# Kernel tuning notes

Measured on AMD Instinct MI355X. Metric: run time of the kernel, lower is better.

The kernel has to match this reference:

```python
import jax, jax.numpy as jnp
import numpy as np

B, S, D = 1, 4096, 768
H = 12
HD = D // H  # 64


def setup_inputs() -> dict:
    key = jax.random.key(0)
    ks = jax.random.split(key, 6)
    sc = 1.0 / np.sqrt(D)
    return {
        "x": jax.random.normal(ks[0], (B, S, D), dtype=jnp.float32),
        "wq": jax.random.normal(ks[1], (D, D), dtype=jnp.float32) * sc,
        "wk": jax.random.normal(ks[2], (D, D), dtype=jnp.float32) * sc,
        "wv": jax.random.normal(ks[3], (D, D), dtype=jnp.float32) * sc,
        "wo": jax.random.normal(ks[4], (D, D), dtype=jnp.float32) * sc,
        "bo": jax.random.normal(ks[5], (D,), dtype=jnp.float32) * 0.02,
    }


def reference(x, wq, wk, wv, wo, bo):
    b, n, _ = x.shape
    # projections (torch Linear: x @ W.T; here weights stored as (d_in, d_out))
    q = (x @ wq).reshape(b, n, H, HD).transpose(0, 2, 1, 3)  # b h n d
    k = (x @ wk).reshape(b, n, H, HD).transpose(0, 2, 1, 3)
    v = (x @ wv).reshape(b, n, H, HD).transpose(0, 2, 1, 3)
    scores = jnp.einsum("bhqd,bhkd->bhqk", q, k)
    causal = jnp.tril(jnp.ones((n, n), dtype=bool))  # True = keep
    scores = jnp.where(causal, scores, -jnp.inf)
    weights = jax.nn.softmax(scores / np.sqrt(HD), axis=-1)
    ctx = jnp.einsum("bhqk,bhkd->bhqd", weights, v)
    ctx = ctx.transpose(0, 2, 1, 3).reshape(b, n, D)
    return ctx @ wo + bo
```

## Files before the change

### kernel.cpp

```cpp
#include <hip/hip_runtime.h>


typedef short bf16x8 __attribute__((ext_vector_type(8)));
typedef float f32x4 __attribute__((ext_vector_type(4)));
typedef unsigned short u16;

static constexpr int S_LEN = 4096;
static constexpr int DIM   = 768;
static constexpr int NH    = 12;
static constexpr float QSCALE = 0.125f * 1.44269504088896340736f;

__device__ inline u16 f2bf(float f) {
  union { float f; unsigned int u; } v; v.f = f;
  unsigned int r = v.u + 0x7FFFu + ((v.u >> 16) & 1u);
  return (u16)(r >> 16);
}

__device__ inline void gload_lds16(const u16* g, u16* s) {
  __builtin_amdgcn_global_load_lds(
      (const __attribute__((address_space(1))) unsigned int*)g,
      (__attribute__((address_space(3))) unsigned int*)s, 16, 0, 0);
}

__global__ __launch_bounds__(256)
void prep_kernel(const float* __restrict__ x, const float* __restrict__ w0,
                 const float* __restrict__ w1, const float* __restrict__ w2,
                 const float* __restrict__ w3, u16* __restrict__ xb,
                 u16* __restrict__ t0, u16* __restrict__ t1,
                 u16* __restrict__ t2, u16* __restrict__ t3) {
  if (blockIdx.z == 4) {
    const size_t n = (size_t)S_LEN * DIM;
    const int id = blockIdx.y * 12 + blockIdx.x;
    const size_t stride = (size_t)144 * 256 * 8;
    for (size_t i = ((size_t)id * 256 + threadIdx.x) * 8; i < n; i += stride) {
      const float4 a = *(const float4*)(x + i);
      const float4 b = *(const float4*)(x + i + 4);
      bf16x8 o;
      o[0] = (short)f2bf(a.x); o[1] = (short)f2bf(a.y);
      o[2] = (short)f2bf(a.z); o[3] = (short)f2bf(a.w);
      o[4] = (short)f2bf(b.x); o[5] = (short)f2bf(b.y);
      o[6] = (short)f2bf(b.z); o[7] = (short)f2bf(b.w);
      *(bf16x8*)(xb + i) = o;
    }
    return;
  }
  __shared__ float T[64][65];
  const float* src; u16* dst;
  switch (blockIdx.z) {
    case 0: src = w0; dst = t0; break;
    case 1: src = w1; dst = t1; break;
    case 2: src = w2; dst = t2; break;
    default: src = w3; dst = t3; break;
  }
  const int k0 = blockIdx.y * 64, n0 = blockIdx.x * 64;
  const int r = threadIdx.x >> 2, c0 = (threadIdx.x & 3) * 16;
#pragma unroll
  for (int i = 0; i < 4; ++i) {
    const float4 v = *(const float4*)(src + (size_t)(k0 + r) * DIM + n0 + c0 + i * 4);
    T[r][c0 + i * 4 + 0] = v.x;
    T[r][c0 + i * 4 + 1] = v.y;
    T[r][c0 + i * 4 + 2] = v.z;
    T[r][c0 + i * 4 + 3] = v.w;
  }
  __syncthreads();
  bf16x8 o0, o1;
#pragma unroll
  for (int i = 0; i < 8; ++i) {
    o0[i] = (short)f2bf(T[c0 + i][r]);
    o1[i] = (short)f2bf(T[c0 + 8 + i][r]);
  }
  *(bf16x8*)(dst + (size_t)(n0 + r) * DIM + k0 + c0) = o0;
  *(bf16x8*)(dst + (size_t)(n0 + r) * DIM + k0 + c0 + 8) = o1;
}

template <int MODE>
__global__ __launch_bounds__(256)
void mfma_gemm_kernel(const u16* __restrict__ A, const u16* __restrict__ Bq,
                      const u16* __restrict__ Bk, const u16* __restrict__ Bv,
                      const float* __restrict__ bias, u16* __restrict__ Qb,
                      u16* __restrict__ Kb, u16* __restrict__ VT,
                      float* __restrict__ Out) {
  constexpr int MT = (MODE == 0) ? 4 : 2;
  constexpr int BM = MT * 32;
  __shared__ __align__(16) u16 Al[BM * 64];
  __shared__ __align__(16) u16 Bl[96 * 64];

  const int tid  = threadIdx.x;
  const int wv   = tid >> 6;
  const int lane = tid & 63;
  const int quad = lane >> 4;
  const int l16  = lane & 15;
  const int wr = wv >> 1, wc = wv & 1;
  const int m0 = blockIdx.y * BM;
  const int n0 = blockIdx.x * 96;

  int wi = 0, nb = n0;
  const u16* BT = Bq;
  if (MODE == 0) {
    wi = n0 / DIM;
    nb = n0 - wi * DIM;
    BT = (wi == 0) ? Bq : (wi == 1) ? Bk : Bv;
  }

  const int sr8 = lane >> 3;
  const int sc  = ((lane & 7) ^ sr8) * 8;
  const int key = l16 & 7;

  const bool swp = (MODE == 1) || (wi < 2);

  f32x4 acc[MT][3] = {};

  for (int k0 = 0; k0 < DIM; k0 += 64) {
    __syncthreads();
#pragma unroll
    for (int j = 0; j < MT; ++j)
      gload_lds16(A + (size_t)(m0 + wv * (BM / 4) + j * 8 + sr8) * DIM + k0 + sc,
                  &Al[(wv * (BM / 4) + j * 8) * 64]);
#pragma unroll
    for (int j = 0; j < 3; ++j)
      gload_lds16(BT + (size_t)(nb + wv * 24 + j * 8 + sr8) * DIM + k0 + sc,
                  &Bl[(wv * 24 + j * 8) * 64]);
    __syncthreads();

#pragma unroll
    for (int kh = 0; kh < 2; ++kh) {
      const int cb = kh * 4;
      bf16x8 af[MT], bfr[3];
#pragma unroll
      for (int mt = 0; mt < MT; ++mt) {
        const int row = wr * (BM / 2) + mt * 16 + l16;
        af[mt] = *(const bf16x8*)&Al[row * 64 + ((cb + quad) ^ key) * 8];
      }
#pragma unroll
      for (int nt = 0; nt < 3; ++nt) {
        const int row = wc * 48 + nt * 16 + l16;
        bfr[nt] = *(const bf16x8*)&Bl[row * 64 + ((cb + quad) ^ key) * 8];
      }
      if (swp) {
#pragma unroll
        for (int mt = 0; mt < MT; ++mt)
#pragma unroll
          for (int nt = 0; nt < 3; ++nt)
            acc[mt][nt] = __builtin_amdgcn_mfma_f32_16x16x32_bf16(
                bfr[nt], af[mt], acc[mt][nt], 0, 0, 0);
      } else {
#pragma unroll
        for (int mt = 0; mt < MT; ++mt)
#pragma unroll
          for (int nt = 0; nt < 3; ++nt)
            acc[mt][nt] = __builtin_amdgcn_mfma_f32_16x16x32_bf16(
                af[mt], bfr[nt], acc[mt][nt], 0, 0, 0);
      }
    }
  }

  if (MODE == 0 && wi >= 2) {
#pragma unroll
    for (int mt = 0; mt < MT; ++mt) {
#pragma unroll
      for (int nt = 0; nt < 3; ++nt) {
        const int row  = m0 + wr * (BM / 2) + mt * 16 + quad * 4;
        const int ncol = nb + wc * 48 + nt * 16 + l16;
        u16 pk[4];
#pragma unroll
        for (int r = 0; r < 4; ++r) pk[r] = f2bf(acc[mt][nt][r]);
        unsigned long long v;
        __builtin_memcpy(&v, pk, 8);
        *(unsigned long long*)(VT + (size_t)ncol * S_LEN + row) = v;
      }
    }
  } else if (MODE == 0) {
    u16* dst = (wi == 0) ? Qb : Kb;
    const float sc_out = (wi == 0) ? QSCALE : 1.0f;
#pragma unroll
    for (int mt = 0; mt < MT; ++mt) {
#pragma unroll
      for (int nt = 0; nt < 3; ++nt) {
        const int row = m0 + wr * (BM / 2) + mt * 16 + l16;
        const int ncb = nb + wc * 48 + nt * 16 + quad * 4;
        u16 pk[4];
#pragma unroll
        for (int r = 0; r < 4; ++r) pk[r] = f2bf(acc[mt][nt][r] * sc_out);
        unsigned long long v;
        __builtin_memcpy(&v, pk, 8);
        *(unsigned long long*)(dst + (size_t)row * DIM + ncb) = v;
      }
    }
  } else {
#pragma unroll
    for (int mt = 0; mt < MT; ++mt) {
#pragma unroll
      for (int nt = 0; nt < 3; ++nt) {
        const int row = m0 + wr * (BM / 2) + mt * 16 + l16;
        const int ncb = n0 + wc * 48 + nt * 16 + quad * 4;
        const float4 b4 = *(const float4*)(bias + ncb);
        float4 ov;
        ov.x = acc[mt][nt][0] + b4.x;
        ov.y = acc[mt][nt][1] + b4.y;
        ov.z = acc[mt][nt][2] + b4.z;
        ov.w = acc[mt][nt][3] + b4.w;
        *(float4*)(Out + (size_t)row * DIM + ncb) = ov;
      }
    }
  }
}

__global__ __launch_bounds__(256)
void attn_mfma_kernel(const u16* __restrict__ Qb, const u16* __restrict__ Kb,
                      const u16* __restrict__ VTb, u16* __restrict__ ctx) {
  __shared__ __align__(16) u16 KVl[128 * 64 + 64 * 128];

  u16* Kl = KVl;
  u16* Vl = KVl + 128 * 64;

  const int tid  = threadIdx.x;
  const int w    = tid >> 6;
  const int lane = tid & 63;
  const int quad = lane >> 4;
  const int l16  = lane & 15;
  const int qw   = w >> 1;
  const int kw   = w & 1;
  const int key  = l16 & 7;

  const int id = blockIdx.x;
  const int rc = id & 7, slot = id >> 3;
  const int h  = (slot < 64) ? rc : 8 + (rc >> 1);
  const int bx = (slot < 64) ? slot : ((rc & 1) * 32 + (slot - 64));

  const int sr8  = lane >> 3;
  const int scK  = ((lane & 7) ^ sr8) * 8;
  const int sr16 = lane >> 4;

#pragma unroll 1
  for (int side = 0; side < 2; ++side) {
    const int qt = side ? (127 - bx) : bx;
    const int q0 = qt * 32;

    const u16* qptr = Qb + (size_t)(q0 + qw * 16 + l16) * DIM + h * 64 + quad * 8;
    const bf16x8 aq0 = *(const bf16x8*)(qptr);
    const bf16x8 aq1 = *(const bf16x8*)(qptr + 32);

    f32x4 o[4] = {};
    float l_s = 0.f;
    const int qg = q0 + qw * 16 + l16;

    const int nkt = qt / 2 + 1;
    const int niter = (nkt + 1) >> 1;
    const int my_last = nkt - 1;

#pragma unroll 1
    for (int i = 0; i < niter; ++i) {
      const int k0g = i * 128;
      __syncthreads();
#pragma unroll
      for (int j = 0; j < 4; ++j)
        gload_lds16(Kb + (size_t)(k0g + w * 32 + j * 8 + sr8) * DIM + h * 64 + scK,
                    &Kl[(w * 32 + j * 8) * 64]);
#pragma unroll
      for (int j = 0; j < 4; ++j) {
        const int vrow = w * 16 + j * 4 + sr16;
        const int vcol = ((lane & 15) ^ (vrow & 7)) * 8;
        gload_lds16(VTb + (size_t)(h * 64 + vrow) * S_LEN + k0g + vcol,
                    &Vl[(w * 16 + j * 4) * 128]);
      }
      __syncthreads();

      const int kt_w = 2 * i + kw;
      if (kt_w < nkt) {
        f32x4 s[4];
#pragma unroll
        for (int t = 0; t < 4; ++t) {
          const int row = kw * 64 + t * 16 + l16;
          const bf16x8 bk0 = *(const bf16x8*)&Kl[row * 64 + (quad ^ key) * 8];
          const bf16x8 bk1 = *(const bf16x8*)&Kl[row * 64 + ((quad ^ 4) ^ key) * 8];
          s[t] = __builtin_amdgcn_mfma_f32_16x16x32_bf16(
              bk0, aq0, f32x4{0.f, 0.f, 0.f, 0.f}, 0, 0, 0);
          s[t] = __builtin_amdgcn_mfma_f32_16x16x32_bf16(bk1, aq1, s[t], 0, 0, 0);
        }

        unsigned Wt[4][2];
        if (kt_w == my_last) {
#pragma unroll
          for (int t = 0; t < 4; ++t) {
            float pr[4];
#pragma unroll
            for (int r = 0; r < 4; ++r) {
              const int kvg = k0g + kw * 64 + t * 16 + quad * 4 + r;
              float p = __builtin_amdgcn_exp2f(s[t][r]);
              if (kvg > qg) p = 0.f;
              l_s += p;
              pr[r] = p;
            }
            asm("v_cvt_pk_bf16_f32 %0, %1, %2" : "=v"(Wt[t][0]) : "v"(pr[0]), "v"(pr[1]));
            asm("v_cvt_pk_bf16_f32 %0, %1, %2" : "=v"(Wt[t][1]) : "v"(pr[2]), "v"(pr[3]));
          }
        } else {
#pragma unroll
          for (int t = 0; t < 4; ++t) {
            float pr[4];
#pragma unroll
            for (int r = 0; r < 4; ++r) {
              const float p = __builtin_amdgcn_exp2f(s[t][r]);
              l_s += p;
              pr[r] = p;
            }
            asm("v_cvt_pk_bf16_f32 %0, %1, %2" : "=v"(Wt[t][0]) : "v"(pr[0]), "v"(pr[1]));
            asm("v_cvt_pk_bf16_f32 %0, %1, %2" : "=v"(Wt[t][1]) : "v"(pr[2]), "v"(pr[3]));
          }
        }

        bf16x8 pa0, pa1;
        {
          unsigned a0 = Wt[0][0], b0 = Wt[1][0];
          unsigned a1 = Wt[0][1], b1 = Wt[1][1];
          asm("v_permlane32_swap_b32 %0, %1" : "+v"(a0), "+v"(b0));
          asm("v_permlane16_swap_b32 %0, %1" : "+v"(a0), "+v"(b0));
          asm("v_permlane32_swap_b32 %0, %1" : "+v"(a1), "+v"(b1));
          asm("v_permlane16_swap_b32 %0, %1" : "+v"(a1), "+v"(b1));
          union { unsigned u[4]; bf16x8 v; } U0;
          U0.u[0] = a0; U0.u[1] = a1; U0.u[2] = b0; U0.u[3] = b1;
          pa0 = U0.v;
          unsigned c0 = Wt[2][0], d0 = Wt[3][0];
          unsigned c1 = Wt[2][1], d1 = Wt[3][1];
          asm("v_permlane32_swap_b32 %0, %1" : "+v"(c0), "+v"(d0));
          asm("v_permlane16_swap_b32 %0, %1" : "+v"(c0), "+v"(d0));
          asm("v_permlane32_swap_b32 %0, %1" : "+v"(c1), "+v"(d1));
          asm("v_permlane16_swap_b32 %0, %1" : "+v"(c1), "+v"(d1));
          union { unsigned u[4]; bf16x8 v; } U1;
          U1.u[0] = c0; U1.u[1] = c1; U1.u[2] = d0; U1.u[3] = d1;
          pa1 = U1.v;
        }

#pragma unroll
        for (int t = 0; t < 4; ++t) {
          const int row = t * 16 + l16;
          const int cc0 = (kw * 8 + quad) ^ key;
          const int cc1 = (kw * 8 + quad + 4) ^ key;
          const bf16x8 vb0 = *(const bf16x8*)&Vl[row * 128 + cc0 * 8];
          const bf16x8 vb1 = *(const bf16x8*)&Vl[row * 128 + cc1 * 8];
          o[t] = __builtin_amdgcn_mfma_f32_16x16x32_bf16(pa0, vb0, o[t], 0, 0, 0);
          o[t] = __builtin_amdgcn_mfma_f32_16x16x32_bf16(pa1, vb1, o[t], 0, 0, 0);
        }
      }
    }

    __syncthreads();
    float* Obuf  = (float*)KVl;
    float* lbufF = Obuf + 5120;
#pragma unroll
    for (int t = 0; t < 4; ++t)
      *(f32x4*)&Obuf[(w * 64 + lane) * 20 + t * 4] = o[t];
    lbufF[w * 64 + lane] = l_s;
    __syncthreads();
#pragma unroll
    for (int t = 0; t < 4; ++t) {
      const f32x4 po = *(const f32x4*)&Obuf[((w ^ 1) * 64 + lane) * 20 + t * 4];
      o[t] += po;
    }
    l_s += lbufF[(w ^ 1) * 64 + lane];

    if (kw == 0) {
      float L = l_s;
      L += __shfl_xor(L, 16);
      L += __shfl_xor(L, 32);
#pragma unroll
      for (int r = 0; r < 4; ++r) {
        const float inv = 1.f / __shfl(L, quad * 4 + r);
        const int row = q0 + qw * 16 + quad * 4 + r;
#pragma unroll
        for (int t = 0; t < 4; ++t)
          ctx[(size_t)row * DIM + h * 64 + t * 16 + l16] = f2bf(o[t][r] * inv);
      }
    }
  }
}

extern "C" void kernel_launch(void* const* d_in, const int* in_sizes, int n_in,
                              void* d_out, int out_size, void* d_ws,
                              size_t ws_size, hipStream_t stream) {
  const float* x  = (const float*)d_in[0];
  const float* wq = (const float*)d_in[1];
  const float* wk = (const float*)d_in[2];
  const float* wv = (const float*)d_in[3];
  const float* wo = (const float*)d_in[4];
  const float* bo = (const float*)d_in[5];

  const size_t n_x = (size_t)S_LEN * DIM;
  const size_t n_w = (size_t)DIM * DIM;
  u16* xb  = (u16*)d_ws;
  u16* wtq = xb + n_x;
  u16* wtk = wtq + n_w;
  u16* wtv = wtk + n_w;
  u16* wto = wtv + n_w;
  u16* Qb  = wto + n_w;
  u16* Kb  = Qb + n_x;
  u16* VTb = Kb + n_x;
  u16* ctx = VTb + n_x;

  prep_kernel<<<dim3(12, 12, 5), 256, 0, stream>>>(
      x, wq, wk, wv, wo, xb, wtq, wtk, wtv, wto);

  mfma_gemm_kernel<0><<<dim3(24, 32), 256, 0, stream>>>(
      xb, wtq, wtk, wtv, nullptr, Qb, Kb, VTb, nullptr);

  attn_mfma_kernel<<<dim3(768), 256, 0, stream>>>(Qb, Kb, VTb, ctx);

  mfma_gemm_kernel<1><<<dim3(8, 64), 256, 0, stream>>>(
      ctx, wto, nullptr, nullptr, bo, nullptr, nullptr, nullptr, (float*)d_out);
}
```

Baseline: 169.1 us.

## Double-buffer K tiles in LDS and prefetch next tile during compute

The attention kernel now keeps two K buffers in LDS and issues the global-to-LDS loads for the next K tile before computing the current one. It replaces __syncthreads with explicit waitcnt plus barrier, waiting only for the current tile's loads via vmcnt(4). It also raises wave priority around the MFMA section. This aims to hide K load latency at the cost of more LDS, which may lower occupancy, and it relies on hand-counted vmcnt values. V is still single-buffered.

```diff
diff --git a/kernel.cpp b/kernel.cpp
--- a/kernel.cpp
+++ b/kernel.cpp
@@ -208,10 +208,8 @@
 __global__ __launch_bounds__(256)
 void attn_mfma_kernel(const u16* __restrict__ Qb, const u16* __restrict__ Kb,
                       const u16* __restrict__ VTb, u16* __restrict__ ctx) {
-  __shared__ __align__(16) u16 KVl[128 * 64 + 64 * 128];
-
-  u16* Kl = KVl;
-  u16* Vl = KVl + 128 * 64;
+  __shared__ __align__(16) u16 KVl[2 * 128 * 64 + 64 * 128];
+  u16* const Vl = KVl + 2 * 128 * 64;
 
   const int tid  = threadIdx.x;
   const int w    = tid >> 6;
@@ -251,11 +249,16 @@
 #pragma unroll 1
     for (int i = 0; i < niter; ++i) {
       const int k0g = i * 128;
-      __syncthreads();
-#pragma unroll
-      for (int j = 0; j < 4; ++j)
-        gload_lds16(Kb + (size_t)(k0g + w * 32 + j * 8 + sr8) * DIM + h * 64 + scK,
-                    &Kl[(w * 32 + j * 8) * 64]);
+      asm volatile("s_waitcnt lgkmcnt(0)" ::: "memory");
+      __builtin_amdgcn_s_barrier();
+
+      u16* const kcur = KVl + (i & 1) * (128 * 64);
+      if (i == 0) {
+#pragma unroll
+        for (int j = 0; j < 4; ++j)
+          gload_lds16(Kb + (size_t)(w * 32 + j * 8 + sr8) * DIM + h * 64 + scK,
+                      &kcur[(w * 32 + j * 8) * 64]);
+      }
 #pragma unroll
       for (int j = 0; j < 4; ++j) {
         const int vrow = w * 16 + j * 4 + sr16;
@@ -263,16 +266,28 @@
         gload_lds16(VTb + (size_t)(h * 64 + vrow) * S_LEN + k0g + vcol,
                     &Vl[(w * 16 + j * 4) * 128]);
       }
-      __syncthreads();
+      const bool more = (i + 1 < niter);
+      if (more) {
+        u16* const knext = KVl + ((i + 1) & 1) * (128 * 64);
+#pragma unroll
+        for (int j = 0; j < 4; ++j)
+          gload_lds16(Kb + (size_t)(k0g + 128 + w * 32 + j * 8 + sr8) * DIM + h * 64 + scK,
+                      &knext[(w * 32 + j * 8) * 64]);
+        asm volatile("s_waitcnt vmcnt(4)" ::: "memory");
+      } else {
+        asm volatile("s_waitcnt vmcnt(0)" ::: "memory");
+      }
+      __builtin_amdgcn_s_barrier();
 
       const int kt_w = 2 * i + kw;
       if (kt_w < nkt) {
+        __builtin_amdgcn_s_setprio(1);
         f32x4 s[4];
 #pragma unroll
         for (int t = 0; t < 4; ++t) {
           const int row = kw * 64 + t * 16 + l16;
-          const bf16x8 bk0 = *(const bf16x8*)&Kl[row * 64 + (quad ^ key) * 8];
-          const bf16x8 bk1 = *(const bf16x8*)&Kl[row * 64 + ((quad ^ 4) ^ key) * 8];
+          const bf16x8 bk0 = *(const bf16x8*)&kcur[row * 64 + (quad ^ key) * 8];
+          const bf16x8 bk1 = *(const bf16x8*)&kcur[row * 64 + ((quad ^ 4) ^ key) * 8];
           s[t] = __builtin_amdgcn_mfma_f32_16x16x32_bf16(
               bk0, aq0, f32x4{0.f, 0.f, 0.f, 0.f}, 0, 0, 0);
           s[t] = __builtin_amdgcn_mfma_f32_16x16x32_bf16(bk1, aq1, s[t], 0, 0, 0);
@@ -341,6 +356,7 @@
           o[t] = __builtin_amdgcn_mfma_f32_16x16x32_bf16(pa0, vb0, o[t], 0, 0, 0);
           o[t] = __builtin_amdgcn_mfma_f32_16x16x32_bf16(pa1, vb1, o[t], 0, 0, 0);
         }
+        __builtin_amdgcn_s_setprio(0);
       }
     }
 
```

New measurement: 165.7 us. 2.0% less time.
